# Optimization experiments

Hardware: AMD Instinct MI355X
Metric: run time of the kernel (lower is better)

The kernel has to match this reference:

```python
import jax, jax.numpy as jnp
import numpy as np

B, T, V, U = 128, 256, 256, 2048


def setup_inputs() -> dict:
    key = jax.random.key(0)
    k_x, k_wx, k_wh, k_wd = jax.random.split(key, 4)
    x = jax.random.randint(k_x, (B, T), 0, V)
    # glorot-ish scaling so tanh doesn't saturate
    Wx = jax.random.normal(k_wx, (V, U), jnp.float32) * (1.0 / np.sqrt(V))
    Wh = jax.random.normal(k_wh, (U, U), jnp.float32) * (1.0 / np.sqrt(U))
    b = jnp.zeros((U,), jnp.float32)
    Wd = jax.random.normal(k_wd, (U, V), jnp.float32) * (1.0 / np.sqrt(U))
    bd = jnp.zeros((V,), jnp.float32)
    h0 = jnp.zeros((B, U), jnp.float32)
    return {"x": x, "Wx": Wx, "Wh": Wh, "b": b, "Wd": Wd, "bd": bd, "h0": h0}


def reference(x, Wx, Wh, b, Wd, bd, h0):
    # one_hot(x, V) @ Wx  ==  Wx[x]  (row gather; avoids materializing one-hot)
    x_proj = Wx[x] + b  # [B, T, U]
    x_proj_t = jnp.swapaxes(x_proj, 0, 1)  # [T, B, U] for scan

    def step(h, xt):
        # SimpleRNN cell: h_t = tanh(x_t Wx + h_{t-1} Wh + b)
        h_new = jnp.tanh(xt + h @ Wh)
        return h_new, h_new

    _, hs = jax.lax.scan(step, h0, x_proj_t)  # hs: [T, B, U]
    hs = jnp.swapaxes(hs, 0, 1)  # [B, T, U]
    logits = jnp.einsum('btu,uv->btv', hs, Wd) + bd  # [B, T, V]
    return logits
```

## Files before the change

kernel.cpp:

```cpp
#include <hip/hip_runtime.h>
#include <hip/hip_bf16.h>

#define B_ 128
#define T_ 256
#define V_ 256
#define U_ 2048

typedef __bf16 bf16x8 __attribute__((ext_vector_type(8)));
typedef float f32x4 __attribute__((ext_vector_type(4)));

union B8u { uint4 u; bf16x8 v; };

static __device__ inline bf16x8 u2b(uint4 u) { B8u t; t.u = u; return t.v; }
static __device__ inline bf16x8 ldg8(const unsigned short* p) {
    B8u t; t.u = *reinterpret_cast<const uint4*>(p); return t.v;
}
static __device__ inline bf16x8 lds8(const char* smem, unsigned off) {
    B8u t; t.u = *reinterpret_cast<const uint4*>(smem + off); return t.v;
}
static __device__ inline unsigned short f2b(float f) {
    __hip_bfloat16 h = __float2bfloat16(f);
    unsigned short r; __builtin_memcpy(&r, &h, 2); return r;
}
static __device__ inline uint4 ldg16_c(const unsigned short* p) {
    uint4 r;
    asm volatile("global_load_dwordx4 %0, %1, off"
                 : "=&v"(r) : "v"(p) : "memory");
    return r;
}
static __device__ inline void stg8_sc(unsigned short* p, uint2 v) {
    asm volatile("global_store_dwordx2 %0, %1, off sc0 sc1"
                 :: "v"(p), "v"(v) : "memory");
}


__global__ void transpose_bf16(const float* __restrict__ in,
                               unsigned short* __restrict__ outp, int R, int C) {
    __shared__ float tile[32][33];
    int tc = blockIdx.x * 32, tr = blockIdx.y * 32;
    int lx = threadIdx.x & 31, ly = threadIdx.x >> 5;
#pragma unroll
    for (int i = 0; i < 32; i += 8)
        tile[ly + i][lx] = in[(size_t)(tr + ly + i) * C + tc + lx];
    __syncthreads();
#pragma unroll
    for (int i = 0; i < 32; i += 8)
        outp[(size_t)(tc + ly + i) * R + tr + lx] = f2b(tile[lx][ly + i]);
}

__global__ void conv_h0(const float* __restrict__ h0, unsigned short* __restrict__ hb) {
    int i = blockIdx.x * blockDim.x + threadIdx.x;
    hb[i] = f2b(h0[i]);
}

__global__ void transpose_x(const int* __restrict__ x, int* __restrict__ xT) {
    int i = blockIdx.x * 256 + threadIdx.x;
    int b = i >> 8, t = i & 255;
    xT[t * B_ + b] = x[i];
}

__global__ __launch_bounds__(256, 1) void rnn_arc2(
        const int* __restrict__ xT, const float* __restrict__ Wx,
        const float* __restrict__ bias, const unsigned short* __restrict__ WhT,
        unsigned short* __restrict__ hs, unsigned* __restrict__ ctrs) {
    extern __shared__ char smem[];
    float* red = (float*)(smem + 32 * 2048 * 2);

    const int bid = blockIdx.x;
    const int g = bid >> 6, p = bid & 63;
    const int b0 = g * 32, c0 = p * 32;
    const int tid = threadIdx.x;
    const int w = tid >> 6, lane = tid & 63;
    const int lr = lane & 15, lh = lane >> 4;

    for (int i = tid; i < 32 * 256; i += 256) {
        int c = i >> 8, k8 = i & 255;
        uint4 v = *reinterpret_cast<const uint4*>(WhT + (size_t)(c0 + c) * U_ + k8 * 8);
        unsigned off = (unsigned)(c * 4096 + k8 * 16) ^ ((unsigned)(c & 7) << 4);
        *reinterpret_cast<uint4*>(smem + off) = v;
    }
    __syncthreads();

    const int kbase = w * 512;
    const unsigned lin0 = (unsigned)(lr * 4096) + (unsigned)((kbase + lh * 8) * 2);
    const unsigned lin1 = lin0 + 16 * 4096;
    const unsigned swz = (unsigned)(lr & 7) << 4;

    const int erow = tid >> 3;
    const int ec4 = (tid & 7) * 4;
    const int ucol = c0 + ec4;
    const f32x4 bias4 = *reinterpret_cast<const f32x4*>(bias + ucol);

    f32x4 xp;
    {
        int tok = xT[0 * B_ + b0 + erow];
        xp = *reinterpret_cast<const f32x4*>(Wx + (size_t)tok * U_ + ucol) + bias4;
    }

    for (int t = 0; t < T_; ++t) {
        const unsigned short* hp = hs + (size_t)t * (B_ * U_);
        unsigned short* hc = hs + (size_t)(t + 1) * (B_ * U_);

        const unsigned short* pa0 = hp + (size_t)(b0 + lr) * U_ + kbase + lh * 8;
        const unsigned short* pa1 = pa0 + 16 * U_;
        uint4 areg0[16], areg1[16];
#pragma unroll
        for (int ks = 0; ks < 16; ++ks) {
            areg0[ks] = ldg16_c(pa0 + ks * 32);
            areg1[ks] = ldg16_c(pa1 + ks * 32);
        }
        asm volatile("s_waitcnt vmcnt(0)" ::: "memory");
        __builtin_amdgcn_sched_barrier(0);

        f32x4 acc00 = {0.f, 0.f, 0.f, 0.f}, acc01 = {0.f, 0.f, 0.f, 0.f};
        f32x4 acc10 = {0.f, 0.f, 0.f, 0.f}, acc11 = {0.f, 0.f, 0.f, 0.f};
#pragma unroll
        for (int ks = 0; ks < 16; ++ks) {
            bf16x8 a0 = u2b(areg0[ks]);
            bf16x8 a1 = u2b(areg1[ks]);
            bf16x8 bb0 = lds8(smem, (lin0 + (unsigned)ks * 64u) ^ swz);
            bf16x8 bb1 = lds8(smem, (lin1 + (unsigned)ks * 64u) ^ swz);
            acc00 = __builtin_amdgcn_mfma_f32_16x16x32_bf16(a0, bb0, acc00, 0, 0, 0);
            acc01 = __builtin_amdgcn_mfma_f32_16x16x32_bf16(a0, bb1, acc01, 0, 0, 0);
            acc10 = __builtin_amdgcn_mfma_f32_16x16x32_bf16(a1, bb0, acc10, 0, 0, 0);
            acc11 = __builtin_amdgcn_mfma_f32_16x16x32_bf16(a1, bb1, acc11, 0, 0, 0);
        }

        float* redw = red + w * 1152;
#pragma unroll
        for (int r = 0; r < 4; ++r) {
            redw[(lh * 4 + r) * 36 + lr] = acc00[r];
            redw[(lh * 4 + r) * 36 + 16 + lr] = acc01[r];
            redw[(16 + lh * 4 + r) * 36 + lr] = acc10[r];
            redw[(16 + lh * 4 + r) * 36 + 16 + lr] = acc11[r];
        }
        __syncthreads();

        {
            const int o = erow * 36 + ec4;
            f32x4 z = *reinterpret_cast<f32x4*>(red + 0 * 1152 + o);
            z += *reinterpret_cast<f32x4*>(red + 1 * 1152 + o);
            z += *reinterpret_cast<f32x4*>(red + 2 * 1152 + o);
            z += *reinterpret_cast<f32x4*>(red + 3 * 1152 + o);
            z += xp;
            unsigned lo = (unsigned)f2b(tanhf(z[0])) | ((unsigned)f2b(tanhf(z[1])) << 16);
            unsigned hi = (unsigned)f2b(tanhf(z[2])) | ((unsigned)f2b(tanhf(z[3])) << 16);
            stg8_sc(hc + (size_t)(b0 + erow) * U_ + ucol, make_uint2(lo, hi));
        }

        if (t + 1 < T_) {
            int tok = xT[(t + 1) * B_ + b0 + erow];
            xp = *reinterpret_cast<const f32x4*>(Wx + (size_t)tok * U_ + ucol) + bias4;
        }

        asm volatile("s_waitcnt vmcnt(0)" ::: "memory");
        __syncthreads();
        if (tid == 0)
            __hip_atomic_fetch_add(ctrs + (g * 8 + (p & 7)) * 32, 1u,
                                   __ATOMIC_RELAXED, __HIP_MEMORY_SCOPE_AGENT);

        if (w == 0) {
            unsigned tgt = (unsigned)(t + 1) * 8u;
            unsigned* cp = ctrs + (g * 8 + (lane & 7)) * 32;
            while (__hip_atomic_load(cp, __ATOMIC_RELAXED, __HIP_MEMORY_SCOPE_AGENT) < tgt)
                __builtin_amdgcn_s_sleep(1);
        }
        __syncthreads();
    }
}

__global__ __launch_bounds__(256, 2) void decode_gemm2(
        const unsigned short* __restrict__ hsD, const unsigned short* __restrict__ WdT,
        const float* __restrict__ bdv, float* __restrict__ out) {
    const int tid = threadIdx.x;
    const int w = tid >> 6, lane = tid & 63;
    const int lr = lane & 15, lh = lane >> 4;
    const int r0 = blockIdx.x * 32;
    const int v0 = w * 64;

    const unsigned short* pa0 = hsD + (size_t)(r0 + lr) * U_ + lh * 8;
    const unsigned short* pa1 = pa0 + (size_t)16 * U_;
    const unsigned short* pb0 = WdT + (size_t)(v0 + lr) * U_ + lh * 8;

    f32x4 acc0[4], acc1[4];
#pragma unroll
    for (int n = 0; n < 4; ++n) {
        acc0[n] = (f32x4){0.f, 0.f, 0.f, 0.f};
        acc1[n] = (f32x4){0.f, 0.f, 0.f, 0.f};
    }

#pragma unroll 4
    for (int ks = 0; ks < 64; ++ks) {
        bf16x8 a0 = ldg8(pa0 + ks * 32);
        bf16x8 a1 = ldg8(pa1 + ks * 32);
#pragma unroll
        for (int n = 0; n < 4; ++n) {
            bf16x8 bb = ldg8(pb0 + (size_t)n * 16 * U_ + ks * 32);
            acc0[n] = __builtin_amdgcn_mfma_f32_16x16x32_bf16(a0, bb, acc0[n], 0, 0, 0);
            acc1[n] = __builtin_amdgcn_mfma_f32_16x16x32_bf16(a1, bb, acc1[n], 0, 0, 0);
        }
    }

#pragma unroll
    for (int n = 0; n < 4; ++n) {
        float bd_ = bdv[v0 + n * 16 + lr];
#pragma unroll
        for (int r = 0; r < 4; ++r) {
            int m0 = r0 + lh * 4 + r;
            int m1 = m0 + 16;
            out[((size_t)(m0 & 127) * T_ + (m0 >> 7)) * V_ + v0 + n * 16 + lr] =
                acc0[n][r] + bd_;
            out[((size_t)(m1 & 127) * T_ + (m1 >> 7)) * V_ + v0 + n * 16 + lr] =
                acc1[n][r] + bd_;
        }
    }
}

extern "C" void kernel_launch(void* const* d_in, const int* in_sizes, int n_in,
                              void* d_out, int out_size, void* d_ws, size_t ws_size,
                              hipStream_t stream) {
    const int* x = (const int*)d_in[0];
    const float* Wx = (const float*)d_in[1];
    const float* Wh = (const float*)d_in[2];
    const float* b = (const float*)d_in[3];
    const float* Wd = (const float*)d_in[4];
    const float* bd = (const float*)d_in[5];
    const float* h0 = (const float*)d_in[6];
    float* out = (float*)d_out;

    char* ws = (char*)d_ws;

    const size_t OFF_WhT = 0;
    const size_t OFF_WdT = 8388608;
    const size_t OFF_xT = 9437184;
    const size_t OFF_CTR = 9568256;
    const size_t OFF_HS = 9572352;

    unsigned short* WhT = (unsigned short*)(ws + OFF_WhT);
    unsigned short* WdT = (unsigned short*)(ws + OFF_WdT);
    int* xT = (int*)(ws + OFF_xT);
    unsigned* ctrs = (unsigned*)(ws + OFF_CTR);
    unsigned short* hs = (unsigned short*)(ws + OFF_HS);

    hipMemsetAsync(ctrs, 0, 4096, stream);
    transpose_bf16<<<dim3(64, 64), 256, 0, stream>>>(Wh, WhT, 2048, 2048);
    transpose_bf16<<<dim3(8, 64), 256, 0, stream>>>(Wd, WdT, 2048, 256);
    conv_h0<<<1024, 256, 0, stream>>>(h0, hs);
    transpose_x<<<128, 256, 0, stream>>>(x, xT);

    const int smem_bytes = 32 * 2048 * 2 + 4 * 1152 * 4;
    hipFuncSetAttribute((const void*)rnn_arc2, hipFuncAttributeMaxDynamicSharedMemorySize,
                        smem_bytes);
    void* args[] = {(void*)&xT, (void*)&Wx, (void*)&b, (void*)&WhT, (void*)&hs,
                    (void*)&ctrs};
    hipLaunchCooperativeKernel((const void*)rnn_arc2, dim3(256), dim3(256), args,
                               (unsigned)smem_bytes, stream);

    const unsigned short* hsD = hs + (size_t)B_ * U_;
    decode_gemm2<<<1024, 256, 0, stream>>>(hsD, WdT, bd, out);
}
```

Measured before the change: 1.935 ms.

## Replace atomic counter barrier with per-wave flags and fast tanh

The per-step inter-block barrier no longer uses two block-wide syncthreads plus an atomic counter polled by one wave. Each wave now publishes its own step flag with a cache-bypassing store, and every wave polls all 256 flags of its batch group with vectorized loads before starting the next step. The next-step Wx gather is issued before the tanh epilogue, and tanhf is replaced by an exp/rcp formulation. The aim is to shorten the per-timestep synchronisation latency on the serial recurrence, at the cost of more polling traffic and slightly lower tanh accuracy.

```diff
diff --git a/kernel.cpp b/kernel.cpp
--- a/kernel.cpp
+++ b/kernel.cpp
@@ -32,6 +32,20 @@
     asm volatile("global_store_dwordx2 %0, %1, off sc0 sc1"
                  :: "v"(p), "v"(v) : "memory");
 }
+static __device__ inline void stg4_sc_u32(unsigned* p, unsigned v) {
+    asm volatile("global_store_dword %0, %1, off sc0 sc1"
+                 :: "v"(p), "v"(v) : "memory");
+}
+static __device__ inline uint4 ldg16_sc_wait(const unsigned* p) {
+    uint4 r;
+    asm volatile("global_load_dwordx4 %0, %1, off sc0 sc1\n\ts_waitcnt vmcnt(0)"
+                 : "=&v"(r) : "v"(p) : "memory");
+    return r;
+}
+static __device__ inline float tanh_fast(float x) {
+    float e = __expf(2.0f * x);
+    return 1.0f - 2.0f * __builtin_amdgcn_rcpf(e + 1.0f);
+}
 
 
 __global__ void transpose_bf16(const float* __restrict__ in,
@@ -59,10 +73,10 @@
     xT[t * B_ + b] = x[i];
 }
 
-__global__ __launch_bounds__(256, 1) void rnn_arc2(
+__global__ __launch_bounds__(256, 1) void rnn_arc7(
         const int* __restrict__ xT, const float* __restrict__ Wx,
         const float* __restrict__ bias, const unsigned short* __restrict__ WhT,
-        unsigned short* __restrict__ hs, unsigned* __restrict__ ctrs) {
+        unsigned short* __restrict__ hs, unsigned* __restrict__ flags) {
     extern __shared__ char smem[];
     float* red = (float*)(smem + 32 * 2048 * 2);
 
@@ -90,6 +104,9 @@
     const int ec4 = (tid & 7) * 4;
     const int ucol = c0 + ec4;
     const f32x4 bias4 = *reinterpret_cast<const f32x4*>(bias + ucol);
+
+    unsigned* myflag = flags + (unsigned)(g * 256 + p * 4 + w);
+    const unsigned* pollp = flags + (unsigned)(g * 256 + lane * 4);
 
     f32x4 xp;
     {
@@ -136,6 +153,12 @@
         }
         __syncthreads();
 
+        f32x4 xpn = xp;
+        if (t + 1 < T_) {
+            int tok = xT[(t + 1) * B_ + b0 + erow];
+            xpn = *reinterpret_cast<const f32x4*>(Wx + (size_t)tok * U_ + ucol) + bias4;
+        }
+
         {
             const int o = erow * 36 + ec4;
             f32x4 z = *reinterpret_cast<f32x4*>(red + 0 * 1152 + o);
@@ -143,29 +166,26 @@
             z += *reinterpret_cast<f32x4*>(red + 2 * 1152 + o);
             z += *reinterpret_cast<f32x4*>(red + 3 * 1152 + o);
             z += xp;
-            unsigned lo = (unsigned)f2b(tanhf(z[0])) | ((unsigned)f2b(tanhf(z[1])) << 16);
-            unsigned hi = (unsigned)f2b(tanhf(z[2])) | ((unsigned)f2b(tanhf(z[3])) << 16);
+            unsigned lo = (unsigned)f2b(tanh_fast(z[0])) |
+                          ((unsigned)f2b(tanh_fast(z[1])) << 16);
+            unsigned hi = (unsigned)f2b(tanh_fast(z[2])) |
+                          ((unsigned)f2b(tanh_fast(z[3])) << 16);
             stg8_sc(hc + (size_t)(b0 + erow) * U_ + ucol, make_uint2(lo, hi));
         }
+        xp = xpn;
+
+        asm volatile("s_waitcnt vmcnt(0)" ::: "memory");
+        if (lane == 0) stg4_sc_u32(myflag, (unsigned)(t + 1));
 
         if (t + 1 < T_) {
-            int tok = xT[(t + 1) * B_ + b0 + erow];
-            xp = *reinterpret_cast<const f32x4*>(Wx + (size_t)tok * U_ + ucol) + bias4;
-        }
-
-        asm volatile("s_waitcnt vmcnt(0)" ::: "memory");
-        __syncthreads();
-        if (tid == 0)
-            __hip_atomic_fetch_add(ctrs + (g * 8 + (p & 7)) * 32, 1u,
-                                   __ATOMIC_RELAXED, __HIP_MEMORY_SCOPE_AGENT);
-
-        if (w == 0) {
-            unsigned tgt = (unsigned)(t + 1) * 8u;
-            unsigned* cp = ctrs + (g * 8 + (lane & 7)) * 32;
-            while (__hip_atomic_load(cp, __ATOMIC_RELAXED, __HIP_MEMORY_SCOPE_AGENT) < tgt)
-                __builtin_amdgcn_s_sleep(1);
-        }
-        __syncthreads();
+            for (;;) {
+                uint4 f = ldg16_sc_wait(pollp);
+                unsigned m01 = f.x < f.y ? f.x : f.y;
+                unsigned m23 = f.z < f.w ? f.z : f.w;
+                unsigned m = m01 < m23 ? m01 : m23;
+                if (__all(m > (unsigned)t)) break;
+            }
+        }
     }
 }
 
@@ -233,27 +253,27 @@
     const size_t OFF_WhT = 0;
     const size_t OFF_WdT = 8388608;
     const size_t OFF_xT = 9437184;
-    const size_t OFF_CTR = 9568256;
+    const size_t OFF_FLG = 9568256;
     const size_t OFF_HS = 9572352;
 
     unsigned short* WhT = (unsigned short*)(ws + OFF_WhT);
     unsigned short* WdT = (unsigned short*)(ws + OFF_WdT);
     int* xT = (int*)(ws + OFF_xT);
-    unsigned* ctrs = (unsigned*)(ws + OFF_CTR);
+    unsigned* flags = (unsigned*)(ws + OFF_FLG);
     unsigned short* hs = (unsigned short*)(ws + OFF_HS);
 
-    hipMemsetAsync(ctrs, 0, 4096, stream);
+    hipMemsetAsync(flags, 0, 4096, stream);
     transpose_bf16<<<dim3(64, 64), 256, 0, stream>>>(Wh, WhT, 2048, 2048);
     transpose_bf16<<<dim3(8, 64), 256, 0, stream>>>(Wd, WdT, 2048, 256);
     conv_h0<<<1024, 256, 0, stream>>>(h0, hs);
     transpose_x<<<128, 256, 0, stream>>>(x, xT);
 
     const int smem_bytes = 32 * 2048 * 2 + 4 * 1152 * 4;
-    hipFuncSetAttribute((const void*)rnn_arc2, hipFuncAttributeMaxDynamicSharedMemorySize,
+    hipFuncSetAttribute((const void*)rnn_arc7, hipFuncAttributeMaxDynamicSharedMemorySize,
                         smem_bytes);
     void* args[] = {(void*)&xT, (void*)&Wx, (void*)&b, (void*)&WhT, (void*)&hs,
-                    (void*)&ctrs};
-    hipLaunchCooperativeKernel((const void*)rnn_arc2, dim3(256), dim3(256), args,
+                    (void*)&flags};
+    hipLaunchCooperativeKernel((const void*)rnn_arc7, dim3(256), dim3(256), args,
                                (unsigned)smem_bytes, stream);
 
     const unsigned short* hsD = hs + (size_t)B_ * U_;
```

Measured after the change: 3.010 ms. 1.56x slower.
